# Kernel tuning notes

Measured on AMD Instinct MI355X. Metric: run time of the kernel, lower is better.

Reference implementation:

```python
import jax, jax.numpy as jnp
import numpy as np

B, S, E, H = 4, 1024, 1024, 16

def setup_inputs() -> dict:
    key = jax.random.key(0)
    ks = jax.random.split(key, 7)
    sc = 0.02
    return {
        "queries": jax.random.normal(ks[0], (B, S, E), jnp.float32),
        "keys": jax.random.normal(ks[1], (B, S, E), jnp.float32),
        "values": jax.random.normal(ks[2], (B, S, E), jnp.float32),
        "Wq_w": jax.random.normal(ks[3], (E, E), jnp.float32) * sc,
        "Wq_b": jax.random.normal(ks[4], (E,), jnp.float32) * sc,
        "Wo_w": jax.random.normal(ks[5], (E, E), jnp.float32) * sc,
        "Wo_b": jax.random.normal(ks[6], (E,), jnp.float32) * sc,
        "num_heads": H,
    }

def reference(queries, keys, values, Wq_w, Wq_b, Wo_w, Wo_b, num_heads):
    b, s, e = queries.shape
    dh = e // num_heads

    def proj_heads(x):
        # NOTE: original module applies Wq to q, k AND v (bug kept faithfully)
        y = x @ Wq_w.T + Wq_b                      # [b, s, e]
        return y.reshape(b, s, num_heads, dh)      # [b, s, h, dh]

    q = proj_heads(queries)
    k = proj_heads(keys)
    v = proj_heads(values)

    scores = jnp.einsum('bqhd,bkhd->bhqk', q, k) / jnp.sqrt(jnp.asarray(dh, q.dtype))
    attn = jax.nn.softmax(scores, axis=-1)         # [b, h, q, k]
    out = jnp.einsum('bhqk,bkhd->bqhd', attn, v)   # [b, s, h, dh]
    out = out.reshape(b, s, e)
    return out @ Wo_w.T + Wo_b
```

## Files before the change

### kernel.cpp

```cpp
#include <hip/hip_runtime.h>
#include <stdint.h>


typedef __attribute__((ext_vector_type(8))) short bf16x8;
typedef __attribute__((ext_vector_type(4))) float f32x4;
typedef __attribute__((ext_vector_type(4))) short short4v;

#define GLOAD_LDS(gp, lp)                                                      \
  __builtin_amdgcn_global_load_lds(                                            \
      (__attribute__((address_space(1))) void*)(gp),                           \
      (__attribute__((address_space(3))) void*)(lp), 16, 0, 0)

__device__ __forceinline__ unsigned short f2bf(float f) {
  union { float f; unsigned u; } v; v.f = f;
  unsigned r = v.u + 0x7FFFu + ((v.u >> 16) & 1u);
  return (unsigned short)(r >> 16);
}
__device__ __forceinline__ unsigned short f2bf_fast(float f) {
  union { float f; unsigned u; } v; v.f = f;
  return (unsigned short)((v.u + 0x8000u) >> 16);
}

template<int CTRL>
__device__ __forceinline__ float dpp_rr(float x) {
  union { float f; int i; } a, r;
  a.f = x;
  r.i = __builtin_amdgcn_update_dpp(0, a.i, CTRL, 0xf, 0xf, false);
  return r.f;
}
__device__ __forceinline__ float rowmax16(float x) {
  x = fmaxf(x, dpp_rr<0x121>(x));
  x = fmaxf(x, dpp_rr<0x122>(x));
  x = fmaxf(x, dpp_rr<0x124>(x));
  x = fmaxf(x, dpp_rr<0x128>(x));
  return x;
}

__global__ void cvt_all(const float* __restrict__ q, const float* __restrict__ k,
                        const float* __restrict__ v, const float* __restrict__ wq,
                        const float* __restrict__ wo, short* __restrict__ dst) {
  int i = blockIdx.x * 256 + threadIdx.x;
  const float* src; int j;
  if (i < 1048576)      { src = q;  j = i; }
  else if (i < 2097152) { src = k;  j = i - 1048576; }
  else if (i < 3145728) { src = v;  j = i - 2097152; }
  else if (i < 3407872) { src = wq; j = i - 3145728; }
  else                  { src = wo; j = i - 3407872; }
  float4 f = reinterpret_cast<const float4*>(src)[j];
  short4v o;
  o.x = (short)f2bf(f.x); o.y = (short)f2bf(f.y);
  o.z = (short)f2bf(f.z); o.w = (short)f2bf(f.w);
  reinterpret_cast<short4v*>(dst)[i] = o;
}

template<int EPI>
__global__ __launch_bounds__(256, 2)
void gemm_bt(const short* __restrict__ A, const short* __restrict__ Bw,
             const float* __restrict__ bias,
             short* __restrict__ qkv, float* __restrict__ outf)
{
  __shared__ short As[128 * 64];
  __shared__ short Bs[128 * 64];
  const int tid  = threadIdx.x;
  const int lane = tid & 63;
  const int g    = lane >> 4;
  const int r7   = lane & 7;
  const int w    = tid >> 6;
  const int wm   = w >> 1, wn = w & 1;

  const int orig = blockIdx.y * 8 + blockIdx.x;
  const int cpx  = (gridDim.x * gridDim.y) >> 3;
  const int t    = (orig & 7) * cpx + (orig >> 3);
  const int m0   = (t >> 3) * 128, n0 = (t & 7) * 128;

  f32x4 acc[4][4] = {};

  for (int k0 = 0; k0 < 1024; k0 += 64) {
#pragma unroll
    for (int c = 0; c < 4; c++) {
      int L   = c * 256 + tid;
      int row = L >> 3;
      int col = ((L & 7) ^ (row & 7)) * 8;
      GLOAD_LDS(A  + (m0 + row) * 1024 + k0 + col, As + L * 8);
      GLOAD_LDS(Bw + (n0 + row) * 1024 + k0 + col, Bs + L * 8);
    }
    __syncthreads();
#pragma unroll
    for (int kk = 0; kk < 2; kk++) {
      bf16x8 av[4], bv[4];
#pragma unroll
      for (int mi = 0; mi < 4; mi++) {
        int row = wm * 64 + mi * 16 + (lane & 15);
        av[mi] = *(const bf16x8*)&As[row * 64 + (((kk * 4 + g) ^ r7) * 8)];
      }
#pragma unroll
      for (int ni = 0; ni < 4; ni++) {
        int row = wn * 64 + ni * 16 + (lane & 15);
        bv[ni] = *(const bf16x8*)&Bs[row * 64 + (((kk * 4 + g) ^ r7) * 8)];
      }
#pragma unroll
      for (int mi = 0; mi < 4; mi++)
#pragma unroll
        for (int ni = 0; ni < 4; ni++)
          acc[mi][ni] = __builtin_amdgcn_mfma_f32_16x16x32_bf16(av[mi], bv[ni], acc[mi][ni], 0, 0, 0);
    }
    __syncthreads();
  }

  if (EPI == 0) {
    const int inp = m0 >> 12;
#pragma unroll
    for (int mi = 0; mi < 4; mi++) {
#pragma unroll
      for (int ni = 0; ni < 4; ni++) {
        const int coll = n0 + wn * 64 + ni * 16 + (lane & 15);
        const float bv = bias[coll];
        const int rbase = m0 + wm * 64 + mi * 16 + (lane >> 4) * 4;
        const int hh = coll >> 6, d = coll & 63;
        if (inp < 2) {
#pragma unroll
          for (int j = 0; j < 4; j++) {
            int rowl = rbase + j;
            int bb = (rowl >> 10) & 3, s = rowl & 1023;
            qkv[(((inp * 4 + bb) * 16 + hh) * 1024 + s) * 64 + d] =
                (short)f2bf(acc[mi][ni][j] + bv);
          }
        } else {
          int bb = (rbase >> 10) & 3, s0 = rbase & 1023;
          short4v o;
          o.x = (short)f2bf(acc[mi][ni][0] + bv);
          o.y = (short)f2bf(acc[mi][ni][1] + bv);
          o.z = (short)f2bf(acc[mi][ni][2] + bv);
          o.w = (short)f2bf(acc[mi][ni][3] + bv);
          *(short4v*)&qkv[8 * 1024 * 1024 + ((bb * 16 + hh) * 64 + d) * 1024 + s0] = o;
        }
      }
    }
  } else {
#pragma unroll
    for (int mi = 0; mi < 4; mi++) {
#pragma unroll
      for (int ni = 0; ni < 4; ni++) {
        const int coll = n0 + wn * 64 + ni * 16 + (lane & 15);
        const float bv = bias[coll];
        const int rbase = m0 + wm * 64 + mi * 16 + (lane >> 4) * 4;
#pragma unroll
        for (int j = 0; j < 4; j++)
          outf[(rbase + j) * 1024 + coll] = acc[mi][ni][j] + bv;
      }
    }
  }
}

__global__ __launch_bounds__(256, 2)
void attn_kernel(const short* __restrict__ qkv, short* __restrict__ O)
{
  __shared__ short Ks[2][64 * 64];
  __shared__ short VTs[2][64 * 64];
  __shared__ short QPs[64 * 64];

  const int tid  = threadIdx.x;
  const int lane = tid & 63;
  const int l15  = lane & 15;
  const int g    = lane >> 4, r7 = lane & 7;
  const int w    = tid >> 6;

  const int t   = (blockIdx.x & 7) * 128 + (blockIdx.x >> 3);
  const int qt  = t & 15, hh = (t >> 4) & 15, bb = t >> 8;
  const int q0  = qt * 64;

  const short* Qg = qkv + (bb * 16 + hh) * 1024 * 64;
  const short* Kg = qkv + 4 * 1024 * 1024 + (bb * 16 + hh) * 1024 * 64;
  const short* Vg = qkv + 8 * 1024 * 1024 + (bb * 16 + hh) * 64 * 1024;

#pragma unroll
  for (int c = 0; c < 2; c++) {
    int L = c * 256 + tid;
    int row = L >> 3;
    int col = ((L & 7) ^ (row & 7)) * 8;
    GLOAD_LDS(Qg + (q0 + row) * 64 + col, QPs + L * 8);
    GLOAD_LDS(Kg + row * 64 + col,        &Ks[0][L * 8]);
    GLOAD_LDS(Vg + row * 1024 + col,      &VTs[0][L * 8]);
  }
  __syncthreads();
  bf16x8 qf[2];
  {
    const int qrow = w * 16 + l15;
    qf[0] = *(const bf16x8*)&QPs[qrow * 64 + ((g ^ r7) * 8)];
    qf[1] = *(const bf16x8*)&QPs[qrow * 64 + (((4 + g) ^ r7) * 8)];
  }
  bf16x8 vf_l = {};
  if (l15 == 0) {
#pragma unroll
    for (int x = 0; x < 8; x++) vf_l[x] = (short)0x3F80;
  }

  const float SC = 0.125f * 1.44269504f;
  float m_run[4];
  f32x4 acc_l = {};
  f32x4 acc_o[4] = {};
#pragma unroll
  for (int j = 0; j < 4; j++) m_run[j] = -1e30f;

  int cur = 0;
  for (int kt = 0; kt < 16; kt++) {
    if (kt < 15) {
#pragma unroll
      for (int c = 0; c < 2; c++) {
        int L = c * 256 + tid;
        int row = L >> 3;
        int col = ((L & 7) ^ (row & 7)) * 8;
        GLOAD_LDS(Kg + ((kt + 1) * 64 + row) * 64 + col, &Ks[cur ^ 1][L * 8]);
        GLOAD_LDS(Vg + row * 1024 + (kt + 1) * 64 + col, &VTs[cur ^ 1][L * 8]);
      }
    }

    f32x4 sa[4] = {};
    __builtin_amdgcn_s_setprio(1);
#pragma unroll
    for (int kk = 0; kk < 2; kk++) {
#pragma unroll
      for (int ni = 0; ni < 4; ni++) {
        int krow = ni * 16 + l15;
        bf16x8 kf = *(const bf16x8*)&Ks[cur][krow * 64 + (((kk * 4 + g) ^ r7) * 8)];
        sa[ni] = __builtin_amdgcn_mfma_f32_16x16x32_bf16(qf[kk], kf, sa[ni], 0, 0, 0);
      }
    }
    __builtin_amdgcn_s_setprio(0);

    float mtl[4];
#pragma unroll
    for (int j = 0; j < 4; j++)
      mtl[j] = fmaxf(fmaxf(sa[0][j], sa[1][j]), fmaxf(sa[2][j], sa[3][j])) * SC;
    float nd = fmaxf(fmaxf(mtl[0] - m_run[0], mtl[1] - m_run[1]),
                     fmaxf(mtl[2] - m_run[2], mtl[3] - m_run[3]));
    if (__any(nd > 8.0f)) {
#pragma unroll
      for (int j = 0; j < 4; j++) {
        float mt = rowmax16(mtl[j]);
        float mn = fmaxf(m_run[j], mt);
        float alpha = __builtin_amdgcn_exp2f(m_run[j] - mn);
        m_run[j] = mn;
        acc_l[j] *= alpha;
#pragma unroll
        for (int di = 0; di < 4; di++) acc_o[di][j] *= alpha;
      }
    }
#pragma unroll
    for (int ni = 0; ni < 4; ni++) {
      int col = ni * 16 + l15;
#pragma unroll
      for (int j = 0; j < 4; j++) {
        int row = w * 16 + g * 4 + j;
        float p = __builtin_amdgcn_exp2f(sa[ni][j] * SC - m_run[j]);
        QPs[row * 64 + (col ^ ((row & 7) << 3))] = (short)f2bf_fast(p);
      }
    }
    __builtin_amdgcn_s_setprio(1);
#pragma unroll
    for (int kk = 0; kk < 2; kk++) {
      int prow = w * 16 + l15;
      bf16x8 pf = *(const bf16x8*)&QPs[prow * 64 + (((kk * 4 + g) ^ r7) * 8)];
      acc_l = __builtin_amdgcn_mfma_f32_16x16x32_bf16(pf, vf_l, acc_l, 0, 0, 0);
#pragma unroll
      for (int di = 0; di < 4; di++) {
        int vrow = di * 16 + l15;
        bf16x8 vf = *(const bf16x8*)&VTs[cur][vrow * 64 + (((kk * 4 + g) ^ r7) * 8)];
        acc_o[di] = __builtin_amdgcn_mfma_f32_16x16x32_bf16(pf, vf, acc_o[di], 0, 0, 0);
      }
    }
    __builtin_amdgcn_s_setprio(0);
    __syncthreads();
    cur ^= 1;
  }

  float linv[4];
#pragma unroll
  for (int j = 0; j < 4; j++) {
    float lv = __shfl(acc_l[j], lane & 48);
    linv[j] = 1.0f / lv;
  }

#pragma unroll
  for (int di = 0; di < 4; di++) {
    int d = hh * 64 + di * 16 + l15;
#pragma unroll
    for (int j = 0; j < 4; j++) {
      int q = q0 + w * 16 + g * 4 + j;
      O[(bb * 1024 + q) * 1024 + d] = (short)f2bf(acc_o[di][j] * linv[j]);
    }
  }
}

extern "C" void kernel_launch(void* const* d_in, const int* in_sizes, int n_in,
                              void* d_out, int out_size, void* d_ws, size_t ws_size,
                              hipStream_t stream)
{
  (void)in_sizes; (void)n_in; (void)out_size; (void)ws_size;
  const float* q    = (const float*)d_in[0];
  const float* k    = (const float*)d_in[1];
  const float* v    = (const float*)d_in[2];
  const float* Wq_w = (const float*)d_in[3];
  const float* Wq_b = (const float*)d_in[4];
  const float* Wo_w = (const float*)d_in[5];
  const float* Wo_b = (const float*)d_in[6];
  float* out = (float*)d_out;

  short* ws   = (short*)d_ws;
  short* Xbf  = ws;
  short* Obf  = ws;
  short* Wqb  = ws + 12582912;
  short* Wob  = ws + 13631488;
  short* qkv  = ws + 14680064;

  cvt_all<<<14336, 256, 0, stream>>>(q, k, v, Wq_w, Wo_w, ws);

  dim3 gp(8, 96);
  gemm_bt<0><<<gp, 256, 0, stream>>>(Xbf, Wqb, Wq_b, qkv, nullptr);

  attn_kernel<<<1024, 256, 0, stream>>>(qkv, Obf);

  dim3 gf(8, 32);
  gemm_bt<1><<<gf, 256, 0, stream>>>(Obf, Wob, Wo_b, nullptr, out);
}
```

Before: 190.4 us.

## Double attention query tile to 128 rows per block for K/V reuse

Each attention block now handles 128 query rows instead of 64. Each wave owns two 16-row query sub-tiles that share every K and V fragment read from LDS, and the grid is halved to 512 blocks. This halves K/V global and LDS traffic per query and doubles MFMA work per LDS read. The cost is more registers per wave for the doubled accumulators, despite launch bounds now asking for 3 blocks per CU, and fewer blocks to spread across the CUs.

```diff
diff --git a/kernel.cpp b/kernel.cpp
--- a/kernel.cpp
+++ b/kernel.cpp
@@ -152,12 +152,12 @@
   }
 }
 
-__global__ __launch_bounds__(256, 2)
+__global__ __launch_bounds__(256, 3)
 void attn_kernel(const short* __restrict__ qkv, short* __restrict__ O)
 {
   __shared__ short Ks[2][64 * 64];
   __shared__ short VTs[2][64 * 64];
-  __shared__ short QPs[64 * 64];
+  __shared__ short QPs[128 * 64];
 
   const int tid  = threadIdx.x;
   const int lane = tid & 63;
@@ -165,29 +165,36 @@
   const int g    = lane >> 4, r7 = lane & 7;
   const int w    = tid >> 6;
 
-  const int t   = (blockIdx.x & 7) * 128 + (blockIdx.x >> 3);
-  const int qt  = t & 15, hh = (t >> 4) & 15, bb = t >> 8;
-  const int q0  = qt * 64;
+  const int t   = (blockIdx.x & 7) * 64 + (blockIdx.x >> 3);
+  const int qt  = t & 7, hh = (t >> 3) & 15, bb = t >> 7;
+  const int q0  = qt * 128;
 
   const short* Qg = qkv + (bb * 16 + hh) * 1024 * 64;
   const short* Kg = qkv + 4 * 1024 * 1024 + (bb * 16 + hh) * 1024 * 64;
   const short* Vg = qkv + 8 * 1024 * 1024 + (bb * 16 + hh) * 64 * 1024;
 
+#pragma unroll
+  for (int c = 0; c < 4; c++) {
+    int L = c * 256 + tid;
+    int row = L >> 3;
+    int col = ((L & 7) ^ (row & 7)) * 8;
+    GLOAD_LDS(Qg + (q0 + row) * 64 + col, QPs + L * 8);
+  }
 #pragma unroll
   for (int c = 0; c < 2; c++) {
     int L = c * 256 + tid;
     int row = L >> 3;
     int col = ((L & 7) ^ (row & 7)) * 8;
-    GLOAD_LDS(Qg + (q0 + row) * 64 + col, QPs + L * 8);
-    GLOAD_LDS(Kg + row * 64 + col,        &Ks[0][L * 8]);
-    GLOAD_LDS(Vg + row * 1024 + col,      &VTs[0][L * 8]);
+    GLOAD_LDS(Kg + row * 64 + col,   &Ks[0][L * 8]);
+    GLOAD_LDS(Vg + row * 1024 + col, &VTs[0][L * 8]);
   }
   __syncthreads();
-  bf16x8 qf[2];
-  {
-    const int qrow = w * 16 + l15;
-    qf[0] = *(const bf16x8*)&QPs[qrow * 64 + ((g ^ r7) * 8)];
-    qf[1] = *(const bf16x8*)&QPs[qrow * 64 + (((4 + g) ^ r7) * 8)];
+  bf16x8 qf[2][2];
+#pragma unroll
+  for (int h = 0; h < 2; h++) {
+    const int qrow = w * 32 + h * 16 + l15;
+    qf[h][0] = *(const bf16x8*)&QPs[qrow * 64 + ((g ^ r7) * 8)];
+    qf[h][1] = *(const bf16x8*)&QPs[qrow * 64 + (((4 + g) ^ r7) * 8)];
   }
   bf16x8 vf_l = {};
   if (l15 == 0) {
@@ -196,11 +203,13 @@
   }
 
   const float SC = 0.125f * 1.44269504f;
-  float m_run[4];
-  f32x4 acc_l = {};
-  f32x4 acc_o[4] = {};
-#pragma unroll
-  for (int j = 0; j < 4; j++) m_run[j] = -1e30f;
+  float m_run[2][4];
+  f32x4 acc_l[2] = {};
+  f32x4 acc_o[2][4] = {};
+#pragma unroll
+  for (int h = 0; h < 2; h++)
+#pragma unroll
+    for (int j = 0; j < 4; j++) m_run[h][j] = -1e30f;
 
   int cur = 0;
   for (int kt = 0; kt < 16; kt++) {
@@ -215,7 +224,7 @@
       }
     }
 
-    f32x4 sa[4] = {};
+    f32x4 sa[2][4] = {};
     __builtin_amdgcn_s_setprio(1);
 #pragma unroll
     for (int kk = 0; kk < 2; kk++) {
@@ -223,50 +232,67 @@
       for (int ni = 0; ni < 4; ni++) {
         int krow = ni * 16 + l15;
         bf16x8 kf = *(const bf16x8*)&Ks[cur][krow * 64 + (((kk * 4 + g) ^ r7) * 8)];
-        sa[ni] = __builtin_amdgcn_mfma_f32_16x16x32_bf16(qf[kk], kf, sa[ni], 0, 0, 0);
+        sa[0][ni] = __builtin_amdgcn_mfma_f32_16x16x32_bf16(qf[0][kk], kf, sa[0][ni], 0, 0, 0);
+        sa[1][ni] = __builtin_amdgcn_mfma_f32_16x16x32_bf16(qf[1][kk], kf, sa[1][ni], 0, 0, 0);
       }
     }
     __builtin_amdgcn_s_setprio(0);
 
-    float mtl[4];
-#pragma unroll
-    for (int j = 0; j < 4; j++)
-      mtl[j] = fmaxf(fmaxf(sa[0][j], sa[1][j]), fmaxf(sa[2][j], sa[3][j])) * SC;
-    float nd = fmaxf(fmaxf(mtl[0] - m_run[0], mtl[1] - m_run[1]),
-                     fmaxf(mtl[2] - m_run[2], mtl[3] - m_run[3]));
+    float mtl[2][4];
+#pragma unroll
+    for (int h = 0; h < 2; h++)
+#pragma unroll
+      for (int j = 0; j < 4; j++)
+        mtl[h][j] = fmaxf(fmaxf(sa[h][0][j], sa[h][1][j]),
+                          fmaxf(sa[h][2][j], sa[h][3][j])) * SC;
+    float nd = -1e30f;
+#pragma unroll
+    for (int h = 0; h < 2; h++)
+#pragma unroll
+      for (int j = 0; j < 4; j++)
+        nd = fmaxf(nd, mtl[h][j] - m_run[h][j]);
     if (__any(nd > 8.0f)) {
 #pragma unroll
-      for (int j = 0; j < 4; j++) {
-        float mt = rowmax16(mtl[j]);
-        float mn = fmaxf(m_run[j], mt);
-        float alpha = __builtin_amdgcn_exp2f(m_run[j] - mn);
-        m_run[j] = mn;
-        acc_l[j] *= alpha;
-#pragma unroll
-        for (int di = 0; di < 4; di++) acc_o[di][j] *= alpha;
-      }
+      for (int h = 0; h < 2; h++)
+#pragma unroll
+        for (int j = 0; j < 4; j++) {
+          float mt = rowmax16(mtl[h][j]);
+          float mn = fmaxf(m_run[h][j], mt);
+          float alpha = __builtin_amdgcn_exp2f(m_run[h][j] - mn);
+          m_run[h][j] = mn;
+          acc_l[h][j] *= alpha;
+#pragma unroll
+          for (int di = 0; di < 4; di++) acc_o[h][di][j] *= alpha;
+        }
     }
 #pragma unroll
     for (int ni = 0; ni < 4; ni++) {
       int col = ni * 16 + l15;
 #pragma unroll
-      for (int j = 0; j < 4; j++) {
-        int row = w * 16 + g * 4 + j;
-        float p = __builtin_amdgcn_exp2f(sa[ni][j] * SC - m_run[j]);
-        QPs[row * 64 + (col ^ ((row & 7) << 3))] = (short)f2bf_fast(p);
-      }
+      for (int h = 0; h < 2; h++)
+#pragma unroll
+        for (int j = 0; j < 4; j++) {
+          int row = w * 32 + h * 16 + g * 4 + j;
+          float p = __builtin_amdgcn_exp2f(sa[h][ni][j] * SC - m_run[h][j]);
+          QPs[row * 64 + (col ^ ((row & 7) << 3))] = (short)f2bf_fast(p);
+        }
     }
     __builtin_amdgcn_s_setprio(1);
 #pragma unroll
     for (int kk = 0; kk < 2; kk++) {
-      int prow = w * 16 + l15;
-      bf16x8 pf = *(const bf16x8*)&QPs[prow * 64 + (((kk * 4 + g) ^ r7) * 8)];
-      acc_l = __builtin_amdgcn_mfma_f32_16x16x32_bf16(pf, vf_l, acc_l, 0, 0, 0);
+      bf16x8 pf[2];
+#pragma unroll
+      for (int h = 0; h < 2; h++) {
+        int prow = w * 32 + h * 16 + l15;
+        pf[h] = *(const bf16x8*)&QPs[prow * 64 + (((kk * 4 + g) ^ r7) * 8)];
+        acc_l[h] = __builtin_amdgcn_mfma_f32_16x16x32_bf16(pf[h], vf_l, acc_l[h], 0, 0, 0);
+      }
 #pragma unroll
       for (int di = 0; di < 4; di++) {
         int vrow = di * 16 + l15;
         bf16x8 vf = *(const bf16x8*)&VTs[cur][vrow * 64 + (((kk * 4 + g) ^ r7) * 8)];
-        acc_o[di] = __builtin_amdgcn_mfma_f32_16x16x32_bf16(pf, vf, acc_o[di], 0, 0, 0);
+        acc_o[0][di] = __builtin_amdgcn_mfma_f32_16x16x32_bf16(pf[0], vf, acc_o[0][di], 0, 0, 0);
+        acc_o[1][di] = __builtin_amdgcn_mfma_f32_16x16x32_bf16(pf[1], vf, acc_o[1][di], 0, 0, 0);
       }
     }
     __builtin_amdgcn_s_setprio(0);
@@ -274,22 +300,26 @@
     cur ^= 1;
   }
 
-  float linv[4];
-#pragma unroll
-  for (int j = 0; j < 4; j++) {
-    float lv = __shfl(acc_l[j], lane & 48);
-    linv[j] = 1.0f / lv;
-  }
-
-#pragma unroll
-  for (int di = 0; di < 4; di++) {
-    int d = hh * 64 + di * 16 + l15;
+  float linv[2][4];
+#pragma unroll
+  for (int h = 0; h < 2; h++)
 #pragma unroll
     for (int j = 0; j < 4; j++) {
-      int q = q0 + w * 16 + g * 4 + j;
-      O[(bb * 1024 + q) * 1024 + d] = (short)f2bf(acc_o[di][j] * linv[j]);
-    }
-  }
+      float lv = __shfl(acc_l[h][j], lane & 48);
+      linv[h][j] = 1.0f / lv;
+    }
+
+#pragma unroll
+  for (int h = 0; h < 2; h++)
+#pragma unroll
+    for (int di = 0; di < 4; di++) {
+      int d = hh * 64 + di * 16 + l15;
+#pragma unroll
+      for (int j = 0; j < 4; j++) {
+        int q = q0 + w * 32 + h * 16 + g * 4 + j;
+        O[(bb * 1024 + q) * 1024 + d] = (short)f2bf(acc_o[h][di][j] * linv[h][j]);
+      }
+    }
 }
 
 extern "C" void kernel_launch(void* const* d_in, const int* in_sizes, int n_in,
@@ -318,7 +348,7 @@
   dim3 gp(8, 96);
   gemm_bt<0><<<gp, 256, 0, stream>>>(Xbf, Wqb, Wq_b, qkv, nullptr);
 
-  attn_kernel<<<1024, 256, 0, stream>>>(qkv, Obf);
+  attn_kernel<<<512, 256, 0, stream>>>(qkv, Obf);
 
   dim3 gf(8, 32);
   gemm_bt<1><<<gf, 256, 0, stream>>>(Obf, Wob, Wo_b, nullptr, out);
```

Result: no change. 190.6 us (+0.1%).
